# Performance work log

Measured on AMD Instinct MI355X. Metric: run time of the kernel, lower is better.

The kernel has to match this reference:

```python
import jax, jax.numpy as jnp
import numpy as np

DIM, NHEADS = 1024, 16
HD = DIM // NHEADS
ROPE_BASE = 10000.0


def rope_cos_sin(seq_len, hd):
    inv_freq = 1.0 / (ROPE_BASE ** (jnp.arange(0, hd, 2, dtype=jnp.float32) / hd))
    t = jnp.arange(seq_len, dtype=jnp.float32)
    freqs = jnp.outer(t, inv_freq)              # [N, hd/2]
    emb = jnp.concatenate([freqs, freqs], -1)   # [N, hd]
    return jnp.cos(emb), jnp.sin(emb)


def rotate_half(x):
    h = x.shape[-1] // 2
    return jnp.concatenate([-x[..., h:], x[..., :h]], -1)


def setup_inputs() -> dict:
    key = jax.random.key(0)
    ks = jax.random.split(key, 5)
    B, N = 1, 2048
    x = jax.random.normal(ks[0], (B, N, DIM), jnp.float32)
    wq = jax.random.normal(ks[1], (DIM, DIM), jnp.float32) * 0.02
    wk = jax.random.normal(ks[2], (DIM, DIM), jnp.float32) * 0.02
    wv = jax.random.normal(ks[3], (DIM, DIM), jnp.float32) * 0.02
    wp = jax.random.normal(ks[4], (DIM, DIM), jnp.float32) * 0.02
    return {"x": x, "wq": wq, "wk": wk, "wv": wv, "wp": wp}


def reference(x, wq, wk, wv, wp):
    B, N, D = x.shape
    H, hd = NHEADS, HD
    # nn.Linear: y = x @ W.T (weights stored [out, in])
    q = (x @ wq.T).reshape(B, N, H, hd)
    k = (x @ wk.T).reshape(B, N, H, hd)
    v = (x @ wv.T).reshape(B, N, H, hd)
    cos, sin = rope_cos_sin(N, hd)
    cos = cos[None, :, None, :]
    sin = sin[None, :, None, :]
    q = q * cos + rotate_half(q) * sin
    k = k * cos + rotate_half(k) * sin
    # SDPA (no mask, non-causal, eval -> no dropout)
    scale = 1.0 / jnp.sqrt(jnp.float32(hd))
    logits = jnp.einsum("bqhd,bkhd->bhqk", q, k) * scale
    attn = jax.nn.softmax(logits, axis=-1)
    out = jnp.einsum("bhqk,bkhd->bqhd", attn, v).reshape(B, N, D)
    return out @ wp.T
```

## Files before the change

### kernel.cpp

```cpp
#include <hip/hip_runtime.h>

typedef short s16x8 __attribute__((ext_vector_type(8)));
typedef float f32x4 __attribute__((ext_vector_type(4)));
typedef float f32x16 __attribute__((ext_vector_type(16)));

__device__ __forceinline__ unsigned short f2bf(float f) {
    unsigned int u = __float_as_uint(f);
    u += 0x7fff + ((u >> 16) & 1);
    return (unsigned short)(u >> 16);
}
__device__ __forceinline__ float bf2f(unsigned short h) {
    return __uint_as_float(((unsigned int)h) << 16);
}
__device__ __forceinline__ f32x4 mfma16(s16x8 a, s16x8 b, f32x4 c) {
    return __builtin_amdgcn_mfma_f32_16x16x32_bf16(a, b, c, 0, 0, 0);
}
__device__ __forceinline__ f32x16 mfma32(s16x8 a, s16x8 b, f32x16 c) {
    return __builtin_amdgcn_mfma_f32_32x32x16_bf16(a, b, c, 0, 0, 0);
}
__device__ __forceinline__ void async16(const void* g, void* l) {
    __builtin_amdgcn_global_load_lds(
        (const __attribute__((address_space(1))) void*)g,
        (__attribute__((address_space(3))) void*)l, 16, 0, 0);
}

#define ROPE_C (-13.287712379549449f / 32.0f)

__global__ __launch_bounds__(256) void convert_all(
    const float* __restrict__ x,  const float* __restrict__ wq,
    const float* __restrict__ wk, const float* __restrict__ wv,
    const float* __restrict__ wp,
    unsigned short* __restrict__ xb, unsigned short* __restrict__ wqkvb,
    unsigned short* __restrict__ wpb)
{
    const size_t XN = 2048u * 1024u, WN = 1024u * 1024u;
    size_t e = ((size_t)blockIdx.x * 256 + threadIdx.x) * 4;
    const float* s; unsigned short* d;
    if (e < XN)                { s = x  + e;               d = xb    + e; }
    else if (e < XN + WN)      { s = wq + (e - XN);        d = wqkvb + (e - XN); }
    else if (e < XN + 2 * WN)  { s = wk + (e - XN - WN);   d = wqkvb + (e - XN); }
    else if (e < XN + 3 * WN)  { s = wv + (e - XN - 2*WN); d = wqkvb + (e - XN); }
    else                       { s = wp + (e - XN - 3*WN); d = wpb   + (e - XN - 3*WN); }
    float4 v = *(const float4*)s;
    ushort4 o;
    o.x = f2bf(v.x); o.y = f2bf(v.y); o.z = f2bf(v.z); o.w = f2bf(v.w);
    *(ushort4*)d = o;
}

template<int BM, int BN, int C32, int ROPE>
__global__ __launch_bounds__(256) void gemm_mfma(
    const unsigned short* __restrict__ A,
    const unsigned short* __restrict__ B,
    void* __restrict__ C, int Ntot)
{
    constexpr int MT = BM / 32, NT = BN / 32;
    __shared__ unsigned short As[BM * 64];
    __shared__ unsigned short Bs[BN * 64];

    const int tid  = threadIdx.x;
    const int wave = tid >> 6, lane = tid & 63;
    const int l16  = lane & 15, quad = lane >> 4;
    const int m0   = blockIdx.y * BM, n0 = blockIdx.x * BN;
    const int wm   = (wave & 1) * (BM / 2), wn = (wave >> 1) * (BN / 2);

    const int srow8 = lane >> 3;
    const int scol  = (lane & 7) * 8;

    f32x4 acc[MT][NT] = {};

    for (int k0 = 0; k0 < 1024; k0 += 64) {
        #pragma unroll
        for (int i = 0; i < BM / 32; i++) {
            int j = wave * (BM / 32) + i;
            async16(A + (size_t)(m0 + j * 8 + srow8) * 1024 + k0 + scol, &As[j * 512]);
        }
        #pragma unroll
        for (int i = 0; i < BN / 32; i++) {
            int j = wave * (BN / 32) + i;
            async16(B + (size_t)(n0 + j * 8 + srow8) * 1024 + k0 + scol, &Bs[j * 512]);
        }
        __syncthreads();

        #pragma unroll
        for (int ks = 0; ks < 2; ks++) {
            s16x8 af[MT], bfr[NT];
            #pragma unroll
            for (int mt = 0; mt < MT; mt++)
                af[mt] = *(const s16x8*)&As[(wm + mt * 16 + l16) * 64 + ks * 32 + quad * 8];
            #pragma unroll
            for (int nt = 0; nt < NT; nt++)
                bfr[nt] = *(const s16x8*)&Bs[(wn + nt * 16 + l16) * 64 + ks * 32 + quad * 8];
            #pragma unroll
            for (int mt = 0; mt < MT; mt++)
                #pragma unroll
                for (int nt = 0; nt < NT; nt++)
                    acc[mt][nt] = mfma16(af[mt], bfr[nt], acc[mt][nt]);
        }
        __syncthreads();
    }

    if constexpr (ROPE) {
        if (n0 < 2048) {
            #pragma unroll
            for (int mt = 0; mt < MT; mt++)
                #pragma unroll
                for (int r = 0; r < 4; r++) {
                    int m = m0 + wm + mt * 16 + quad * 4 + r;
                    #pragma unroll
                    for (int nt = 0; nt < 2; nt++) {
                        int i = nt * 16 + l16;
                        float ang = (float)m * exp2f((float)i * ROPE_C);
                        float c, s;
                        sincosf(ang, &c, &s);
                        float e0 = acc[mt][nt][r], e1 = acc[mt][nt + 2][r];
                        acc[mt][nt][r]     = e0 * c + e1 * s;
                        acc[mt][nt + 2][r] = e1 * c - e0 * s;
                    }
                }
        }
    }

    #pragma unroll
    for (int mt = 0; mt < MT; mt++)
        #pragma unroll
        for (int nt = 0; nt < NT; nt++)
            #pragma unroll
            for (int r = 0; r < 4; r++) {
                int m = m0 + wm + mt * 16 + quad * 4 + r;
                int n = n0 + wn + nt * 16 + l16;
                size_t idx = (size_t)m * Ntot + n;
                if (C32) ((float*)C)[idx] = acc[mt][nt][r];
                else     ((unsigned short*)C)[idx] = f2bf(acc[mt][nt][r]);
            }
}

__global__ __launch_bounds__(256, 4) void attn_part(
    const unsigned short* __restrict__ qkv,
    unsigned short* __restrict__ Opart, float* __restrict__ Lpart)
{
    const int h  = blockIdx.y;
    const int q0 = blockIdx.x * 128;
    const int ks = blockIdx.z;
    const int tid  = threadIdx.x;
    const int wave = tid >> 6, lane = tid & 63;
    const int l32  = lane & 31, half = lane >> 5;

    __shared__ unsigned short Ks[64][72];
    __shared__ unsigned short Vt[64][72];
    __shared__ unsigned short Ps[4][32][72];

    const unsigned short* qp = qkv + (size_t)(q0 + wave * 32 + l32) * 3072 + h * 64 + half * 8;
    s16x8 qb[4];
    #pragma unroll
    for (int c = 0; c < 4; c++)
        qb[c] = *(const s16x8*)(qp + c * 16);

    f32x16 o0 = {}, o1 = {};
    float lsum = 0.f;

    for (int t = 0; t < 8; t++) {
        const int kt = ks * 512 + t * 64;

        if (tid < 128) {
            int g  = tid & 15;
            int d0 = (tid >> 4) * 8;
            const unsigned short* gv = qkv + (size_t)(kt + 4 * g) * 3072 + 2048 + h * 64 + d0;
            unsigned short a0[8], a1[8], a2[8], a3[8];
            *(uint4*)a0 = *(const uint4*)gv;
            *(uint4*)a1 = *(const uint4*)(gv + 3072);
            *(uint4*)a2 = *(const uint4*)(gv + 6144);
            *(uint4*)a3 = *(const uint4*)(gv + 9216);
            #pragma unroll
            for (int d = 0; d < 8; d++) {
                ushort4 w;
                w.x = a0[d]; w.y = a1[d]; w.z = a2[d]; w.w = a3[d];
                *(ushort4*)&Vt[d0 + d][4 * g] = w;
            }
        } else {
            int u = tid - 128;
            int key = u & 63;
            int dh = (u >> 6) * 32;
            const unsigned short* gk = qkv + (size_t)(kt + key) * 3072 + 1024 + h * 64 + dh;
            const uint4* g4 = (const uint4*)gk;
            uint4 k0 = g4[0], k1 = g4[1], k2 = g4[2], k3 = g4[3];
            *(uint4*)&Ks[key][dh]      = k0;
            *(uint4*)&Ks[key][dh + 8]  = k1;
            *(uint4*)&Ks[key][dh + 16] = k2;
            *(uint4*)&Ks[key][dh + 24] = k3;
        }
        __syncthreads();

        #pragma unroll
        for (int g = 0; g < 2; g++) {
            f32x16 s = {};
            #pragma unroll
            for (int c = 0; c < 4; c++) {
                s16x8 ka = *(const s16x8*)&Ks[g * 32 + l32][c * 16 + half * 8];
                s = mfma32(ka, qb[c], s);
            }
            #pragma unroll
            for (int c = 0; c < 4; c++) {
                float e0 = __expf(s[4 * c + 0] * 0.125f);
                float e1 = __expf(s[4 * c + 1] * 0.125f);
                float e2 = __expf(s[4 * c + 2] * 0.125f);
                float e3 = __expf(s[4 * c + 3] * 0.125f);
                lsum += (e0 + e1) + (e2 + e3);
                ushort4 w;
                w.x = f2bf(e0); w.y = f2bf(e1); w.z = f2bf(e2); w.w = f2bf(e3);
                *(ushort4*)&Ps[wave][l32][g * 32 + c * 8 + half * 4] = w;
            }
        }

        #pragma unroll
        for (int c = 0; c < 4; c++) {
            s16x8 pa = *(const s16x8*)&Ps[wave][l32][c * 16 + half * 8];
            s16x8 v0 = *(const s16x8*)&Vt[l32][c * 16 + half * 8];
            s16x8 v1 = *(const s16x8*)&Vt[32 + l32][c * 16 + half * 8];
            o0 = mfma32(pa, v0, o0);
            o1 = mfma32(pa, v1, o1);
        }
        __syncthreads();
    }

    lsum += __shfl_xor(lsum, 32, 64);

    const int mq = q0 + wave * 32;
    unsigned short* opBase = Opart + (size_t)ks * 2048 * 1024;
    #pragma unroll
    for (int r = 0; r < 16; r++) {
        int qr = (r & 3) + 8 * (r >> 2) + 4 * half;
        unsigned short* op = opBase + (size_t)(mq + qr) * 1024 + h * 64;
        op[l32]      = f2bf(o0[r]);
        op[32 + l32] = f2bf(o1[r]);
    }
    if (half == 0)
        Lpart[((size_t)ks * 2048 + mq + l32) * 16 + h] = lsum;
}

__global__ __launch_bounds__(256) void combine(
    const unsigned short* __restrict__ Opart, const float* __restrict__ Lpart,
    unsigned short* __restrict__ ab)
{
    size_t e = ((size_t)blockIdx.x * 256 + threadIdx.x) * 4;
    int tok = (int)(e >> 10);
    int h = (int)((e & 1023) >> 6);
    float l = 0.f;
    #pragma unroll
    for (int s = 0; s < 4; s++)
        l += Lpart[((size_t)s * 2048 + tok) * 16 + h];
    float inv = 1.0f / l;
    float a0 = 0.f, a1 = 0.f, a2 = 0.f, a3 = 0.f;
    #pragma unroll
    for (int s = 0; s < 4; s++) {
        ushort4 n = *(const ushort4*)(Opart + (size_t)s * 2048 * 1024 + e);
        a0 += bf2f(n.x); a1 += bf2f(n.y); a2 += bf2f(n.z); a3 += bf2f(n.w);
    }
    ushort4 w;
    w.x = f2bf(a0 * inv);
    w.y = f2bf(a1 * inv);
    w.z = f2bf(a2 * inv);
    w.w = f2bf(a3 * inv);
    *(ushort4*)(ab + e) = w;
}

extern "C" void kernel_launch(void* const* d_in, const int* in_sizes, int n_in,
                              void* d_out, int out_size, void* d_ws, size_t ws_size,
                              hipStream_t stream)
{
    const float* x  = (const float*)d_in[0];
    const float* wq = (const float*)d_in[1];
    const float* wk = (const float*)d_in[2];
    const float* wv = (const float*)d_in[3];
    const float* wp = (const float*)d_in[4];

    unsigned short* xb    = (unsigned short*)d_ws;
    unsigned short* wqkvb = xb    + 2u * 1024 * 1024;
    unsigned short* wpb   = wqkvb + 3u * 1024 * 1024;
    unsigned short* qkv   = wpb   + 1u * 1024 * 1024;
    unsigned short* ab    = qkv   + 2048u * 3072;
    unsigned short* Opart = ab    + 2u * 1024 * 1024;
    float* Lpart = (float*)(Opart + 4u * 2048 * 1024);

    convert_all<<<6144, 256, 0, stream>>>(x, wq, wk, wv, wp, xb, wqkvb, wpb);
    gemm_mfma<64, 128, 0, 1><<<dim3(24, 32), 256, 0, stream>>>(
        xb, wqkvb, qkv, 3072);
    attn_part<<<dim3(16, 16, 4), 256, 0, stream>>>(qkv, Opart, Lpart);
    combine<<<2048, 256, 0, stream>>>(Opart, Lpart, ab);
    gemm_mfma<64, 64, 1, 0><<<dim3(16, 32), 256, 0, stream>>>(
        ab, wpb, d_out, 1024);
}
```

Measured before the change: 155.9 us.

## Keep softmax probabilities in registers via permlane swap; enlarge QKV GEMM tile

The attention kernel no longer writes the exponentiated scores to a shared-memory P buffer and reads them back. Instead it packs them to bf16 in registers and uses v_permlane32_swap to rearrange lanes into the MFMA A-operand layout, feeding the PV MFMAs directly. This removes the Ps LDS traffic and its footprint, which may also help occupancy. Separately, the QKV projection GEMM switches to 128x128 tiles with half as many blocks in y, trading parallelism for more reuse per block.

```diff
diff --git a/kernel.cpp b/kernel.cpp
--- a/kernel.cpp
+++ b/kernel.cpp
@@ -3,6 +3,7 @@
 typedef short s16x8 __attribute__((ext_vector_type(8)));
 typedef float f32x4 __attribute__((ext_vector_type(4)));
 typedef float f32x16 __attribute__((ext_vector_type(16)));
+typedef unsigned int u32x4 __attribute__((ext_vector_type(4)));
 
 __device__ __forceinline__ unsigned short f2bf(float f) {
     unsigned int u = __float_as_uint(f);
@@ -11,6 +12,9 @@
 }
 __device__ __forceinline__ float bf2f(unsigned short h) {
     return __uint_as_float(((unsigned int)h) << 16);
+}
+__device__ __forceinline__ unsigned pack2bf(float lo, float hi) {
+    return (unsigned)f2bf(lo) | ((unsigned)f2bf(hi) << 16);
 }
 __device__ __forceinline__ f32x4 mfma16(s16x8 a, s16x8 b, f32x4 c) {
     return __builtin_amdgcn_mfma_f32_16x16x32_bf16(a, b, c, 0, 0, 0);
@@ -147,7 +151,6 @@
 
     __shared__ unsigned short Ks[64][72];
     __shared__ unsigned short Vt[64][72];
-    __shared__ unsigned short Ps[4][32][72];
 
     const unsigned short* qp = qkv + (size_t)(q0 + wave * 32 + l32) * 3072 + h * 64 + half * 8;
     s16x8 qb[4];
@@ -199,25 +202,27 @@
                 s = mfma32(ka, qb[c], s);
             }
             #pragma unroll
-            for (int c = 0; c < 4; c++) {
-                float e0 = __expf(s[4 * c + 0] * 0.125f);
-                float e1 = __expf(s[4 * c + 1] * 0.125f);
-                float e2 = __expf(s[4 * c + 2] * 0.125f);
-                float e3 = __expf(s[4 * c + 3] * 0.125f);
-                lsum += (e0 + e1) + (e2 + e3);
-                ushort4 w;
-                w.x = f2bf(e0); w.y = f2bf(e1); w.z = f2bf(e2); w.w = f2bf(e3);
-                *(ushort4*)&Ps[wave][l32][g * 32 + c * 8 + half * 4] = w;
-            }
-        }
-
-        #pragma unroll
-        for (int c = 0; c < 4; c++) {
-            s16x8 pa = *(const s16x8*)&Ps[wave][l32][c * 16 + half * 8];
-            s16x8 v0 = *(const s16x8*)&Vt[l32][c * 16 + half * 8];
-            s16x8 v1 = *(const s16x8*)&Vt[32 + l32][c * 16 + half * 8];
-            o0 = mfma32(pa, v0, o0);
-            o1 = mfma32(pa, v1, o1);
+            for (int f = 0; f < 2; f++) {
+                float e[8];
+                #pragma unroll
+                for (int j = 0; j < 8; j++) {
+                    e[j] = __expf(s[8 * f + j] * 0.125f);
+                    lsum += e[j];
+                }
+                unsigned w0 = pack2bf(e[0], e[1]);
+                unsigned w1 = pack2bf(e[2], e[3]);
+                unsigned w2 = pack2bf(e[4], e[5]);
+                unsigned w3 = pack2bf(e[6], e[7]);
+                asm("v_permlane32_swap_b32 %0, %1" : "+v"(w0), "+v"(w2));
+                asm("v_permlane32_swap_b32 %0, %1" : "+v"(w1), "+v"(w3));
+                u32x4 wv; wv.x = w0; wv.y = w1; wv.z = w2; wv.w = w3;
+                s16x8 pa = __builtin_bit_cast(s16x8, wv);
+                const int c = 2 * g + f;
+                s16x8 v0 = *(const s16x8*)&Vt[l32][c * 16 + half * 8];
+                s16x8 v1 = *(const s16x8*)&Vt[32 + l32][c * 16 + half * 8];
+                o0 = mfma32(pa, v0, o0);
+                o1 = mfma32(pa, v1, o1);
+            }
         }
         __syncthreads();
     }
@@ -282,7 +287,7 @@
     float* Lpart = (float*)(Opart + 4u * 2048 * 1024);
 
     convert_all<<<6144, 256, 0, stream>>>(x, wq, wk, wv, wp, xb, wqkvb, wpb);
-    gemm_mfma<64, 128, 0, 1><<<dim3(24, 32), 256, 0, stream>>>(
+    gemm_mfma<128, 128, 0, 1><<<dim3(24, 16), 256, 0, stream>>>(
         xb, wqkvb, qkv, 3072);
     attn_part<<<dim3(16, 16, 4), 256, 0, stream>>>(qkv, Opart, Lpart);
     combine<<<2048, 256, 0, stream>>>(Opart, Lpart, ab);
```

Measured after the change: 177.5 us. 1.14x slower.
